# Kernel tuning notes

Measured on AMD Instinct MI355X. Metric: run time of the kernel, lower is better.

Reference implementation:

```python
import jax, jax.numpy as jnp
import numpy as np

EPS = 1.0
POS_WEIGHT = 1.0
REDUCTION = 'mean'

N, D = 8192, 128
NUM_CLASSES = 32


def setup_inputs() -> dict:
    key = jax.random.key(0)
    k1, k2 = jax.random.split(key)
    ys = jax.random.normal(k1, (N, D), dtype=jnp.float32)
    labels = jax.random.randint(k2, (N,), 0, NUM_CLASSES, dtype=jnp.int64)
    return {"ys": ys, "labels": labels}


def reference(ys, labels):
    n = ys.shape[0]
    # Pairwise squared distances via one GEMM: ||a||^2 + ||b||^2 - 2 a.b
    sq = jnp.sum(ys * ys, axis=-1)                      # [N]
    d2 = sq[:, None] + sq[None, :] - 2.0 * (ys @ ys.T)  # [N, N]
    d2 = jnp.maximum(d2, 0.0)
    pair = jnp.triu(jnp.ones((n, n), dtype=bool), k=1)  # i < j, each unordered pair once
    same = labels[:, None] == labels[None, :]
    # positive-pair term: pos_weight * squared distance
    pos = POS_WEIGHT * d2
    # negative-pair term: clip(eps - sqrt(d2), 0)^2 ; guard sqrt(0) for unused entries
    neg_mask = pair & (~same)
    d = jnp.sqrt(jnp.where(neg_mask, d2, 1.0))
    neg = jnp.clip(EPS - d, 0.0) ** 2
    terms = jnp.where(same, pos, neg) * pair.astype(ys.dtype)
    loss = jnp.sum(terms)
    if REDUCTION == 'mean':
        loss = loss / (n * (n - 1) / 2)
    return loss.reshape(1)
```

## Files before the change

kernel.cpp:

```cpp
#include <hip/hip_runtime.h>
#include <stdint.h>
#include <math.h>

#define NN 8192
#define DD 128
#define NB 64
#define NBLK (NB * (NB + 1) / 2)
#define NC 32
#define NPB 256
#define RPB 32
#define TOTBLK (NBLK + NC)
#define SCALE (2.0f / ((float)NN * (float)(NN - 1)))

typedef __attribute__((ext_vector_type(4))) float f32x4;


__device__ __forceinline__ uint32_t pk4_fp8(float f0, float f1, float f2, float f3) {
    int d = __builtin_amdgcn_cvt_pk_fp8_f32(f0, f1, 0, false);
    d = __builtin_amdgcn_cvt_pk_fp8_f32(f2, f3, d, true);
    return (uint32_t)d;
}

__global__ __launch_bounds__(256) void prep_kernel(const float* __restrict__ ys,
                                                   const int* __restrict__ lab,
                                                   uint32_t* __restrict__ a8,
                                                   uint32_t* __restrict__ b8,
                                                   float* __restrict__ sq,
                                                   float* __restrict__ clspart,
                                                   float* __restrict__ out) {
    int b = blockIdx.x, t = threadIdx.x;
    __shared__ float cls[4][NC][DD];
    __shared__ int slab[RPB];

#pragma unroll
    for (int i = 0; i < 16; ++i) ((float4*)cls)[i * 256 + t] = make_float4(0.f, 0.f, 0.f, 0.f);
    if (t < RPB) slab[t] = lab[b * RPB + t];

#pragma unroll
    for (int u = 0; u < 2; ++u) {
        int rloc = (t >> 4) + u * 16;
        int c8 = t & 15;
        int row = b * RPB + rloc;
        const float* base = ys + (size_t)row * DD + c8 * 8;
        float4 v0 = *(const float4*)base;
        float4 v1 = *(const float4*)(base + 4);
        uint2 outB = make_uint2(pk4_fp8(v0.x, v0.y, v0.z, v0.w),
                                pk4_fp8(v1.x, v1.y, v1.z, v1.w));
        uint2 outA = make_uint2(pk4_fp8(-2.f * v0.x, -2.f * v0.y, -2.f * v0.z, -2.f * v0.w),
                                pk4_fp8(-2.f * v1.x, -2.f * v1.y, -2.f * v1.z, -2.f * v1.w));
        size_t off = (size_t)(b * 2 + u) * 2048 + (c8 >> 2) * 512 + (c8 & 3) * 128 + (rloc & 15) * 8;
        *(uint2*)((char*)b8 + off) = outB;
        *(uint2*)((char*)a8 + off) = outA;
        float s = v0.x * v0.x + v0.y * v0.y + v0.z * v0.z + v0.w * v0.w
                + v1.x * v1.x + v1.y * v1.y + v1.z * v1.z + v1.w * v1.w;
        s += __shfl_xor(s, 1); s += __shfl_xor(s, 2);
        s += __shfl_xor(s, 4); s += __shfl_xor(s, 8);
        if (c8 == 0) sq[row] = s;
    }
    __syncthreads();

    {
        int g = t >> 6, col0 = (t & 63) * 2;
#pragma unroll
        for (int rr = 0; rr < 8; ++rr) {
            int rloc = g * 8 + rr;
            float2 v = *(const float2*)(ys + (size_t)(b * RPB + rloc) * DD + col0);
            int lb = slab[rloc];
            cls[g][lb][col0]     += v.x;
            cls[g][lb][col0 + 1] += v.y;
        }
    }
    __syncthreads();
#pragma unroll
    for (int i = 0; i < 4; ++i) {
        int idx = i * 256 + t;
        float4 s0 = ((const float4*)cls[0])[idx];
        float4 s1 = ((const float4*)cls[1])[idx];
        float4 s2 = ((const float4*)cls[2])[idx];
        float4 s3 = ((const float4*)cls[3])[idx];
        ((float4*)(clspart + (size_t)b * NC * DD))[idx] =
            make_float4((s0.x + s1.x) + (s2.x + s3.x), (s0.y + s1.y) + (s2.y + s3.y),
                        (s0.z + s1.z) + (s2.z + s3.z), (s0.w + s1.w) + (s2.w + s3.w));
    }
    if (b == 0 && t == 0) out[0] = 0.f;
}

__global__ __launch_bounds__(256) void loss_kernel(const uint32_t* __restrict__ a8,
                                                   const uint32_t* __restrict__ b8,
                                                   const float* __restrict__ sq,
                                                   const int* __restrict__ lab,
                                                   const float* __restrict__ clspart,
                                                   const float* __restrict__ ys,
                                                   float* __restrict__ out) {
    int p = blockIdx.x, t = threadIdx.x;

    if (p < NC) {
        __shared__ float sp[2][DD];
        __shared__ float redc[4], reds[4], red2[2];
        int col = t & 127, half = t >> 7;
        float S0 = 0.f, S1 = 0.f, S2 = 0.f, S3 = 0.f;
        const float* cp = clspart + (size_t)half * 128 * NC * DD + p * DD + col;
#pragma unroll 8
        for (int pb = 0; pb < 128; pb += 4) {
            S0 += cp[(size_t)(pb + 0) * NC * DD];
            S1 += cp[(size_t)(pb + 1) * NC * DD];
            S2 += cp[(size_t)(pb + 2) * NC * DD];
            S3 += cp[(size_t)(pb + 3) * NC * DD];
        }
        sp[half][col] = (S0 + S1) + (S2 + S3);

        float cnt = 0.f, ssq = 0.f;
        for (int rr = t; rr < NN; rr += 256) {
            if (lab[rr] == p) { cnt += 1.f; ssq += sq[rr]; }
        }
#pragma unroll
        for (int off = 32; off >= 1; off >>= 1) {
            cnt += __shfl_down(cnt, off);
            ssq += __shfl_down(ssq, off);
        }
        if ((t & 63) == 0) { redc[t >> 6] = cnt; reds[t >> 6] = ssq; }
        __syncthreads();

        float s2 = 0.f;
        if (t < DD) { float Sc = sp[0][t] + sp[1][t]; s2 = Sc * Sc; }
#pragma unroll
        for (int off = 32; off >= 1; off >>= 1) s2 += __shfl_down(s2, off);
        if (t < 128 && (t & 63) == 0) red2[t >> 6] = s2;
        __syncthreads();
        if (t == 0) {
            float c = redc[0] + redc[1] + redc[2] + redc[3];
            float s = reds[0] + reds[1] + reds[2] + reds[3];
            atomicAdd(out, (c * s - (red2[0] + red2[1])) * SCALE);
        }
        return;
    }

    int pt = p - NC;
    int q = (NBLK - 1) - pt;
    int r = (int)((sqrtf(8.0f * (float)q + 1.0f) - 1.0f) * 0.5f);
    while (r * (r + 1) / 2 > q) --r;
    while ((r + 1) * (r + 2) / 2 <= q) ++r;
    int bi = (NB - 1) - r;
    int bj = (NB - 1) - (q - r * (r + 1) / 2);
    int i0 = bi * 128, j0 = bj * 128;

    int wave = t >> 6, lane = t & 63;
    int wm = wave >> 1, wn = wave & 1;
    int lr = lane & 15, lg = lane >> 4;

    f32x4 acc[4][4];
#pragma unroll
    for (int m = 0; m < 4; ++m)
#pragma unroll
        for (int n = 0; n < 4; ++n) acc[m][n] = (f32x4){0.f, 0.f, 0.f, 0.f};

    const char* pa = (const char*)a8 + ((size_t)(i0 >> 4) + wm * 4) * 2048 + lg * 128 + lr * 8;
    const char* pbp = (const char*)b8 + ((size_t)(j0 >> 4) + wn * 4) * 2048 + lg * 128 + lr * 8;

#pragma unroll
    for (int ks = 0; ks < 4; ++ks) {
        long af[4], bf[4];
#pragma unroll
        for (int m = 0; m < 4; ++m) af[m] = *(const long*)(pa + m * 2048 + ks * 512);
#pragma unroll
        for (int n = 0; n < 4; ++n) bf[n] = *(const long*)(pbp + n * 2048 + ks * 512);
#pragma unroll
        for (int m = 0; m < 4; ++m)
#pragma unroll
            for (int n = 0; n < 4; ++n)
                acc[m][n] = __builtin_amdgcn_mfma_f32_16x16x32_fp8_fp8(af[m], bf[n], acc[m][n], 0, 0, 0);
    }

    float msi = fminf(sq[i0 + lane * 2], sq[i0 + lane * 2 + 1]);
    float msj = fminf(sq[j0 + lane * 2], sq[j0 + lane * 2 + 1]);
#pragma unroll
    for (int off = 32; off >= 1; off >>= 1) {
        msi = fminf(msi, __shfl_xor(msi, off));
        msj = fminf(msj, __shfl_xor(msj, off));
    }
    float mn = acc[0][0][0];
#pragma unroll
    for (int m = 0; m < 4; ++m)
#pragma unroll
        for (int n = 0; n < 4; ++n)
#pragma unroll
            for (int qq = 0; qq < 4; ++qq) mn = fminf(mn, acc[m][n][qq]);

    if (__any(mn + msi + msj < 20.0f)) {
        float ns = 0.f;
#pragma unroll
        for (int m = 0; m < 4; ++m)
#pragma unroll
            for (int n = 0; n < 4; ++n)
#pragma unroll
                for (int qq = 0; qq < 4; ++qq) {
                    int i = i0 + wm * 64 + m * 16 + lg * 4 + qq;
                    int j = j0 + wn * 64 + n * 16 + lr;
                    float d2a = acc[m][n][qq] + sq[i] + sq[j];
                    if (d2a < 20.0f && i < j && lab[i] != lab[j]) {
                        float d2e = 0.f;
                        for (int d = 0; d < DD; ++d) {
                            float df = ys[(size_t)i * DD + d] - ys[(size_t)j * DD + d];
                            d2e += df * df;
                        }
                        if (d2e < 1.0f) { float e = 1.0f - sqrtf(d2e); ns += e * e; }
                    }
                }
        if (ns != 0.f) atomicAdd(out, ns * SCALE);
    }
}

extern "C" void kernel_launch(void* const* d_in, const int* in_sizes, int n_in,
                              void* d_out, int out_size, void* d_ws, size_t ws_size,
                              hipStream_t stream) {
    const float* ys = (const float*)d_in[0];
    const int* lab = (const int*)d_in[1];
    float* out = (float*)d_out;

    char* w = (char*)d_ws;
    uint32_t* a8    = (uint32_t*)(w);
    uint32_t* b8    = (uint32_t*)(w + 1048576);
    float* sq       = (float*)(w + 2097152);
    float* clspart  = (float*)(w + 2129920);

    prep_kernel<<<NPB, 256, 0, stream>>>(ys, lab, a8, b8, sq, clspart, out);
    loss_kernel<<<TOTBLK, 256, 0, stream>>>(a8, b8, sq, lab, clspart, ys, out);
}
```

Before: 32.17 us.

## Repack fp8 operands for 16-byte loads and precompute per-tile min norms

Result: slower. 35.42 us (+10.1%).

```diff
diff --git a/kernel.cpp b/kernel.cpp
--- a/kernel.cpp
+++ b/kernel.cpp
@@ -27,15 +27,19 @@
                                                    uint32_t* __restrict__ b8,
                                                    float* __restrict__ sq,
                                                    float* __restrict__ clspart,
+                                                   float* __restrict__ tminpart,
                                                    float* __restrict__ out) {
     int b = blockIdx.x, t = threadIdx.x;
     __shared__ float cls[4][NC][DD];
     __shared__ int slab[RPB];
+    __shared__ int tmn;
 
 #pragma unroll
     for (int i = 0; i < 16; ++i) ((float4*)cls)[i * 256 + t] = make_float4(0.f, 0.f, 0.f, 0.f);
     if (t < RPB) slab[t] = lab[b * RPB + t];
-
+    if (t == 0) tmn = 0x7f800000;
+
+    float myMin = 1e30f;
 #pragma unroll
     for (int u = 0; u < 2; ++u) {
         int rloc = (t >> 4) + u * 16;
@@ -48,16 +52,19 @@
                                 pk4_fp8(v1.x, v1.y, v1.z, v1.w));
         uint2 outA = make_uint2(pk4_fp8(-2.f * v0.x, -2.f * v0.y, -2.f * v0.z, -2.f * v0.w),
                                 pk4_fp8(-2.f * v1.x, -2.f * v1.y, -2.f * v1.z, -2.f * v1.w));
-        size_t off = (size_t)(b * 2 + u) * 2048 + (c8 >> 2) * 512 + (c8 & 3) * 128 + (rloc & 15) * 8;
+        size_t off = (size_t)(b * 2 + u) * 2048 + (c8 >> 3) * 1024 + (c8 & 3) * 256
+                   + (rloc & 15) * 16 + ((c8 >> 2) & 1) * 8;
         *(uint2*)((char*)b8 + off) = outB;
         *(uint2*)((char*)a8 + off) = outA;
         float s = v0.x * v0.x + v0.y * v0.y + v0.z * v0.z + v0.w * v0.w
                 + v1.x * v1.x + v1.y * v1.y + v1.z * v1.z + v1.w * v1.w;
         s += __shfl_xor(s, 1); s += __shfl_xor(s, 2);
         s += __shfl_xor(s, 4); s += __shfl_xor(s, 8);
-        if (c8 == 0) sq[row] = s;
-    }
+        if (c8 == 0) { sq[row] = s; myMin = fminf(myMin, s); }
+    }
+    if ((t & 15) == 0) atomicMin(&tmn, __float_as_int(myMin));
     __syncthreads();
+    if (t == 0) tminpart[b] = __int_as_float(tmn);
 
     {
         int g = t >> 6, col0 = (t & 63) * 2;
@@ -90,6 +97,7 @@
                                                    const float* __restrict__ sq,
                                                    const int* __restrict__ lab,
                                                    const float* __restrict__ clspart,
+                                                   const float* __restrict__ tminpart,
                                                    const float* __restrict__ ys,
                                                    float* __restrict__ out) {
     int p = blockIdx.x, t = threadIdx.x;
@@ -147,6 +155,22 @@
     int wave = t >> 6, lane = t & 63;
     int wm = wave >> 1, wn = wave & 1;
     int lr = lane & 15, lg = lane >> 4;
+    int lo16 = lg * 256 + lr * 16;
+
+    float4 ti = ((const float4*)tminpart)[bi];
+    float4 tj = ((const float4*)tminpart)[bj];
+
+    const char* pa = (const char*)a8 + ((size_t)bi * 8 + wm * 4) * 2048 + lo16;
+    const char* pbp = (const char*)b8 + ((size_t)bj * 8 + wn * 4) * 2048 + lo16;
+
+    long2 A0[4], A1[4], B0[4], B1[4];
+#pragma unroll
+    for (int m = 0; m < 4; ++m) {
+        A0[m] = *(const long2*)(pa + m * 2048);
+        A1[m] = *(const long2*)(pa + m * 2048 + 1024);
+        B0[m] = *(const long2*)(pbp + m * 2048);
+        B1[m] = *(const long2*)(pbp + m * 2048 + 1024);
+    }
 
     f32x4 acc[4][4];
 #pragma unroll
@@ -154,30 +178,23 @@
 #pragma unroll
         for (int n = 0; n < 4; ++n) acc[m][n] = (f32x4){0.f, 0.f, 0.f, 0.f};
 
-    const char* pa = (const char*)a8 + ((size_t)(i0 >> 4) + wm * 4) * 2048 + lg * 128 + lr * 8;
-    const char* pbp = (const char*)b8 + ((size_t)(j0 >> 4) + wn * 4) * 2048 + lg * 128 + lr * 8;
-
-#pragma unroll
-    for (int ks = 0; ks < 4; ++ks) {
-        long af[4], bf[4];
-#pragma unroll
-        for (int m = 0; m < 4; ++m) af[m] = *(const long*)(pa + m * 2048 + ks * 512);
-#pragma unroll
-        for (int n = 0; n < 4; ++n) bf[n] = *(const long*)(pbp + n * 2048 + ks * 512);
-#pragma unroll
-        for (int m = 0; m < 4; ++m)
-#pragma unroll
-            for (int n = 0; n < 4; ++n)
-                acc[m][n] = __builtin_amdgcn_mfma_f32_16x16x32_fp8_fp8(af[m], bf[n], acc[m][n], 0, 0, 0);
-    }
-
-    float msi = fminf(sq[i0 + lane * 2], sq[i0 + lane * 2 + 1]);
-    float msj = fminf(sq[j0 + lane * 2], sq[j0 + lane * 2 + 1]);
-#pragma unroll
-    for (int off = 32; off >= 1; off >>= 1) {
-        msi = fminf(msi, __shfl_xor(msi, off));
-        msj = fminf(msj, __shfl_xor(msj, off));
-    }
+#pragma unroll
+    for (int m = 0; m < 4; ++m)
+#pragma unroll
+        for (int n = 0; n < 4; ++n) {
+            acc[m][n] = __builtin_amdgcn_mfma_f32_16x16x32_fp8_fp8(A0[m].x, B0[n].x, acc[m][n], 0, 0, 0);
+            acc[m][n] = __builtin_amdgcn_mfma_f32_16x16x32_fp8_fp8(A0[m].y, B0[n].y, acc[m][n], 0, 0, 0);
+        }
+#pragma unroll
+    for (int m = 0; m < 4; ++m)
+#pragma unroll
+        for (int n = 0; n < 4; ++n) {
+            acc[m][n] = __builtin_amdgcn_mfma_f32_16x16x32_fp8_fp8(A1[m].x, B1[n].x, acc[m][n], 0, 0, 0);
+            acc[m][n] = __builtin_amdgcn_mfma_f32_16x16x32_fp8_fp8(A1[m].y, B1[n].y, acc[m][n], 0, 0, 0);
+        }
+
+    float tb = fminf(fminf(ti.x, ti.y), fminf(ti.z, ti.w))
+             + fminf(fminf(tj.x, tj.y), fminf(tj.z, tj.w));
     float mn = acc[0][0][0];
 #pragma unroll
     for (int m = 0; m < 4; ++m)
@@ -186,7 +203,7 @@
 #pragma unroll
             for (int qq = 0; qq < 4; ++qq) mn = fminf(mn, acc[m][n][qq]);
 
-    if (__any(mn + msi + msj < 20.0f)) {
+    if (__any(mn + tb < 20.0f)) {
         float ns = 0.f;
 #pragma unroll
         for (int m = 0; m < 4; ++m)
@@ -196,14 +213,16 @@
                 for (int qq = 0; qq < 4; ++qq) {
                     int i = i0 + wm * 64 + m * 16 + lg * 4 + qq;
                     int j = j0 + wn * 64 + n * 16 + lr;
-                    float d2a = acc[m][n][qq] + sq[i] + sq[j];
-                    if (d2a < 20.0f && i < j && lab[i] != lab[j]) {
-                        float d2e = 0.f;
-                        for (int d = 0; d < DD; ++d) {
-                            float df = ys[(size_t)i * DD + d] - ys[(size_t)j * DD + d];
-                            d2e += df * df;
+                    if (i < j) {
+                        float d2a = acc[m][n][qq] + sq[i] + sq[j];
+                        if (d2a < 20.0f && lab[i] != lab[j]) {
+                            float d2e = 0.f;
+                            for (int d = 0; d < DD; ++d) {
+                                float df = ys[(size_t)i * DD + d] - ys[(size_t)j * DD + d];
+                                d2e += df * df;
+                            }
+                            if (d2e < 1.0f) { float e = 1.0f - sqrtf(d2e); ns += e * e; }
                         }
-                        if (d2e < 1.0f) { float e = 1.0f - sqrtf(d2e); ns += e * e; }
                     }
                 }
         if (ns != 0.f) atomicAdd(out, ns * SCALE);
@@ -218,11 +237,12 @@
     float* out = (float*)d_out;
 
     char* w = (char*)d_ws;
-    uint32_t* a8    = (uint32_t*)(w);
-    uint32_t* b8    = (uint32_t*)(w + 1048576);
-    float* sq       = (float*)(w + 2097152);
-    float* clspart  = (float*)(w + 2129920);
-
-    prep_kernel<<<NPB, 256, 0, stream>>>(ys, lab, a8, b8, sq, clspart, out);
-    loss_kernel<<<TOTBLK, 256, 0, stream>>>(a8, b8, sq, lab, clspart, ys, out);
-}
+    uint32_t* a8     = (uint32_t*)(w);
+    uint32_t* b8     = (uint32_t*)(w + 1048576);
+    float* sq        = (float*)(w + 2097152);
+    float* clspart   = (float*)(w + 2129920);
+    float* tminpart  = (float*)(w + 6324224);
+
+    prep_kernel<<<NPB, 256, 0, stream>>>(ys, lab, a8, b8, sq, clspart, tminpart, out);
+    loss_kernel<<<TOTBLK, 256, 0, stream>>>(a8, b8, sq, lab, clspart, tminpart, ys, out);
+}
```
